# Performance work log

Measured on AMD Instinct MI355X. Metric: run time of the kernel, lower is better.

Reference implementation:

```python
import jax, jax.numpy as jnp
import numpy as np

D, H = 2048, 16
Q_RANK, KV_RANK = 1536, 512
NOPE, ROPE_D, V_D = 128, 64, 128
QK_D = NOPE + ROPE_D  # 192
S, B = 2048, 1
THETA = 10000.0
EPS = 1e-5


def rmsnorm(x, w, eps=EPS):
    return x * jax.lax.rsqrt(jnp.mean(x * x, -1, keepdims=True) + eps) * w


def rope_cos_sin(s, d, theta=THETA):
    inv = 1.0 / (theta ** (jnp.arange(0, d, 2, dtype=jnp.float32) / d))
    f = jnp.arange(s, dtype=jnp.float32)[:, None] * inv[None, :]  # [s, d//2]
    emb = jnp.concatenate([f, f], -1)  # [s, d]
    return jnp.cos(emb), jnp.sin(emb)


def apply_rope(x, cos, sin):
    # DeepSeek-V3 variant: de-interleave consecutive pairs into [even | odd] halves first
    b, h, s, d = x.shape
    x = x.reshape(b, h, s, d // 2, 2).transpose(0, 1, 2, 4, 3).reshape(b, h, s, d)
    x1, x2 = jnp.split(x, 2, -1)
    rot = jnp.concatenate([-x2, x1], -1)
    return x * cos + rot * sin


def setup_inputs() -> dict:
    key = jax.random.key(0)
    ks = jax.random.split(key, 10)
    s = 0.02
    return {
        "x": jax.random.normal(ks[0], (S, B, D), jnp.float32),
        "norm1_w": jnp.ones((D,), jnp.float32),
        "q_a_w": jax.random.normal(ks[1], (D, Q_RANK), jnp.float32) * s,
        "q_a_ln_w": jnp.ones((Q_RANK,), jnp.float32),
        "q_b_w": jax.random.normal(ks[2], (Q_RANK, H * QK_D), jnp.float32) * s,
        "kv_a_w": jax.random.normal(ks[3], (D, KV_RANK + ROPE_D), jnp.float32) * s,
        "kv_a_ln_w": jnp.ones((KV_RANK,), jnp.float32),
        "kv_b_w": jax.random.normal(ks[4], (KV_RANK, H * (NOPE + V_D)), jnp.float32) * s,
        "o_w": jax.random.normal(ks[5], (H * V_D, D), jnp.float32) * s,
        "norm2_w": jnp.ones((D,), jnp.float32),
        "ffn_w1": jax.random.normal(ks[6], (D, 4 * D), jnp.float32) * s,
        "ffn_b1": jnp.zeros((4 * D,), jnp.float32),
        "ffn_w2": jax.random.normal(ks[7], (4 * D, D), jnp.float32) * s,
        "ffn_b2": jnp.zeros((D,), jnp.float32),
    }


def reference(x, norm1_w, q_a_w, q_a_ln_w, q_b_w, kv_a_w, kv_a_ln_w, kv_b_w, o_w,
              norm2_w, ffn_w1, ffn_b1, ffn_w2, ffn_b2):
    # x: [S, B, D] (block transposes to [B, S, D] before MLA)
    hs = jnp.swapaxes(rmsnorm(x, norm1_w), 0, 1)  # [B, S, D]
    b, s, _ = hs.shape

    # --- MLA: low-rank Q and KV with decoupled RoPE ---
    q = rmsnorm(hs @ q_a_w, q_a_ln_w) @ q_b_w                    # [B, S, H*192]
    q = q.reshape(b, s, H, QK_D).transpose(0, 2, 1, 3)           # [B, H, S, 192]
    q_nope, q_pe = q[..., :NOPE], q[..., NOPE:]

    kv_a = hs @ kv_a_w                                           # [B, S, 576]
    c_kv, k_pe = kv_a[..., :KV_RANK], kv_a[..., KV_RANK:]        # [B,S,512], [B,S,64]
    kv = rmsnorm(c_kv, kv_a_ln_w) @ kv_b_w                       # [B, S, H*256]
    kv = kv.reshape(b, s, H, NOPE + V_D).transpose(0, 2, 1, 3)   # [B, H, S, 256]
    k_nope, v = kv[..., :NOPE], kv[..., NOPE:]

    cos, sin = rope_cos_sin(s, ROPE_D)
    q_pe = apply_rope(q_pe, cos, sin)                            # [B, H, S, 64]
    k_pe = apply_rope(k_pe[:, None, :, :], cos, sin)             # [B, 1, S, 64]

    q_full = jnp.concatenate([q_nope, q_pe], -1)                 # [B, H, S, 192]
    k_full = jnp.concatenate([k_nope, jnp.broadcast_to(k_pe, (b, H, s, ROPE_D))], -1)

    scores = jnp.einsum('bhqd,bhkd->bhqk', q_full, k_full) * (1.0 / np.sqrt(QK_D))
    causal = jnp.tril(jnp.ones((s, s), bool))
    scores = jnp.where(causal, scores, jnp.finfo(scores.dtype).min)
    attn = jax.nn.softmax(scores, -1)
    out = jnp.einsum('bhqk,bhkd->bhqd', attn, v)                 # [B, H, S, 128]
    out = out.transpose(0, 2, 1, 3).reshape(b, s, H * V_D) @ o_w # [B, S, D]

    x = x + jnp.swapaxes(out, 0, 1)                              # residual, back to [S,B,D]

    # --- FFN (exact GELU) ---
    h2 = rmsnorm(x, norm2_w)
    ffn = jax.nn.gelu(h2 @ ffn_w1 + ffn_b1, approximate=False) @ ffn_w2 + ffn_b2
    return x + ffn
```

## Files before the change

### kernel.cpp

```cpp
#include <hip/hip_runtime.h>
#include <hip/hip_bf16.h>

typedef __hip_bfloat16 bf16;
using bf16x8 = __attribute__((ext_vector_type(8))) __bf16;
using f32x4  = __attribute__((ext_vector_type(4))) float;

#define S_   2048
#define D_   2048
#define H_   16
#define QR_  1536
#define KVR_ 512
#define NOPE_ 128
#define ROPE_ 64
#define VD_  128
#define QKD_ 192
#define EPS_ 1e-5f
#define QKVN 2112

#define GLDS16(g, l) \
    __builtin_amdgcn_global_load_lds((const __attribute__((address_space(1))) void*)(g), \
                                     (__attribute__((address_space(3))) void*)(l), 16, 0, 0)

#define PIPE_WAIT4 asm volatile("s_waitcnt vmcnt(4)\n\ts_barrier" ::: "memory")
#define PIPE_WAIT0 asm volatile("s_waitcnt vmcnt(0)\n\ts_barrier" ::: "memory")

__global__ __launch_bounds__(256) void gemm_k(
    const bf16* __restrict__ A, const bf16* __restrict__ BT, void* __restrict__ Cv,
    const float* __restrict__ bias, const float* __restrict__ res,
    int M, int N, int K, int lda, int ldb, int ldc,
    long long strideA, long long strideB, long long strideC,
    int mode, int causal, int ksplit, int kchunk)
{
    int bn = blockIdx.x, bm = blockIdx.y;
    int bzC = blockIdx.z;
    int bz = bzC, kc = 0;
    if (ksplit > 1) { kc = bzC % ksplit; bz = bzC / ksplit; }
    if (causal == 1 && bn > bm) return;
    A  += (size_t)bz * strideA;
    BT += (size_t)bz * strideB;

    int k_end = K;
    if (causal == 2) { int kl = (bm + 1) * 128; if (kl < k_end) k_end = kl; }
    int k_begin = kc * kchunk;
    if (k_begin + kchunk < k_end) k_end = k_begin + kchunk;
    if (k_begin >= k_end) return;
    int nIter = (k_end - k_begin) >> 5;

    __shared__ bf16 sA[3 * 128 * 32];
    __shared__ bf16 sB[3 * 128 * 32];

    int tid  = threadIdx.x;
    int lane = tid & 63, wave = tid >> 6;
    int wr = wave >> 1, wc = wave & 1;
    int fr = lane & 15, fq = lane >> 4;

    int row0 = bm * 128, col0 = bn * 128;

    int srow = wave * 16 + (lane >> 2);
    int sko  = (lane & 3) * 8;
    const bf16* ga0 = A + (size_t)(row0 + srow) * lda + sko;
    const bf16* ga1 = ga0 + (size_t)64 * lda;
    int bn0 = col0 + srow;      if (bn0 > N - 1) bn0 = N - 1;
    int bn1 = col0 + srow + 64; if (bn1 > N - 1) bn1 = N - 1;
    const bf16* gb0 = BT + (size_t)bn0 * ldb + sko;
    const bf16* gb1 = BT + (size_t)bn1 * ldb + sko;
    bf16* lA0 = &sA[(wave * 16) * 32];
    bf16* lA1 = &sA[(64 + wave * 16) * 32];
    bf16* lB0 = &sB[(wave * 16) * 32];
    bf16* lB1 = &sB[(64 + wave * 16) * 32];

#define STAGE(ofs, k0) do {                  \
        GLDS16(ga0 + (k0), lA0 + (ofs));     \
        GLDS16(ga1 + (k0), lA1 + (ofs));     \
        GLDS16(gb0 + (k0), lB0 + (ofs));     \
        GLDS16(gb1 + (k0), lB1 + (ofs));     \
    } while (0)

    f32x4 acc[4][4] = {};

#define COMPUTE(ofs) do {                                                           \
        bf16x8 af[4], bv[4];                                                        \
        _Pragma("unroll")                                                           \
        for (int i = 0; i < 4; ++i)                                                 \
            af[i] = *(const bf16x8*)&sA[(ofs) + (wr*64 + i*16 + fr)*32 + fq*8];     \
        _Pragma("unroll")                                                           \
        for (int j = 0; j < 4; ++j)                                                 \
            bv[j] = *(const bf16x8*)&sB[(ofs) + (wc*64 + j*16 + fr)*32 + fq*8];     \
        _Pragma("unroll")                                                           \
        for (int i = 0; i < 4; ++i)                                                 \
            _Pragma("unroll")                                                       \
            for (int j = 0; j < 4; ++j)                                             \
                acc[i][j] = __builtin_amdgcn_mfma_f32_16x16x32_bf16(af[i], bv[j], acc[i][j], 0, 0, 0); \
    } while (0)

    STAGE(0, k_begin);
    if (nIter > 1) STAGE(4096, k_begin + 32);

    int curo = 0, pfo = 8192;
    int it = 0;
    for (; it < nIter - 1; ++it) {
        PIPE_WAIT4;
        if (it + 2 < nIter) STAGE(pfo, k_begin + (it + 2) * 32);
        COMPUTE(curo);
        curo += 4096; if (curo == 12288) curo = 0;
        pfo  += 4096; if (pfo  == 12288) pfo  = 0;
    }
    PIPE_WAIT0;
    COMPUTE(curo);
#undef STAGE
#undef COMPUTE

    #pragma unroll
    for (int i = 0; i < 4; ++i) {
        #pragma unroll
        for (int j = 0; j < 4; ++j) {
            int gc = col0 + wc*64 + j*16 + fr;
            if (gc >= N) continue;
            #pragma unroll
            for (int r = 0; r < 4; ++r) {
                int gr = row0 + wr*64 + i*16 + fq*4 + r;
                float v = acc[i][j][r];
                size_t off = (size_t)bzC * strideC + (size_t)gr * ldc + gc;
                if (mode == 0 || mode == 6) {
                    ((float*)Cv)[off] = v;
                } else if (mode == 1) {
                    ((bf16*)Cv)[off] = __float2bfloat16(v);
                } else if (mode == 2) {
                    ((float*)Cv)[off] = v + res[(size_t)gr * ldc + gc];
                } else if (mode == 3) {
                    float t = v + bias[gc];
                    t = 0.5f * t * (1.0f + erff(t * 0.70710678118654752f));
                    ((bf16*)Cv)[off] = __float2bfloat16(t);
                } else {
                    ((float*)Cv)[off] = v + bias[gc] + res[(size_t)gr * ldc + gc];
                }
            }
        }
    }
}

__global__ __launch_bounds__(256) void red_k(const float* __restrict__ part,
        long long pstride4, int nch, const float* __restrict__ res,
        const float* __restrict__ bias, long long cols4,
        float* __restrict__ dstF, bf16* __restrict__ dstB, long long n4)
{
    long long i = (long long)blockIdx.x * 256 + threadIdx.x;
    long long stride = (long long)gridDim.x * 256;
    for (; i < n4; i += stride) {
        float4 v = ((const float4*)part)[i];
        for (int k = 1; k < nch; ++k) {
            float4 p = ((const float4*)part)[i + k * pstride4];
            v.x += p.x; v.y += p.y; v.z += p.z; v.w += p.w;
        }
        if (res) {
            float4 rr = ((const float4*)res)[i];
            v.x += rr.x; v.y += rr.y; v.z += rr.z; v.w += rr.w;
        }
        if (bias) {
            float4 b = ((const float4*)bias)[i % cols4];
            v.x += b.x; v.y += b.y; v.z += b.z; v.w += b.w;
        }
        if (dstB) {
            ushort4 o;
            bf16 t0 = __float2bfloat16(v.x); o.x = *(unsigned short*)&t0;
            bf16 t1 = __float2bfloat16(v.y); o.y = *(unsigned short*)&t1;
            bf16 t2 = __float2bfloat16(v.z); o.z = *(unsigned short*)&t2;
            bf16 t3 = __float2bfloat16(v.w); o.w = *(unsigned short*)&t3;
            ((ushort4*)dstB)[i] = o;
        } else {
            ((float4*)dstF)[i] = v;
        }
    }
}

__global__ __launch_bounds__(128) void pv_red(const float* __restrict__ part,
                                              bf16* __restrict__ ao, int grp)
{
    int r = blockIdx.x, head = blockIdx.y, d = threadIdx.x;
    int nv = ((r >> 7) + 4) >> 2;
    const float* p = part + ((size_t)head * 4) * S_ * VD_ + (size_t)r * VD_ + d;
    float s = 0.f;
    for (int k = 0; k < nv; ++k) s += p[(size_t)k * S_ * VD_];
    ao[(size_t)r * (H_ * VD_) + grp * 1024 + head * VD_ + d] = __float2bfloat16(s);
}

__global__ __launch_bounds__(256) void transpose_w(const float* __restrict__ in,
                                                   bf16* __restrict__ out, int R, int C)
{
    __shared__ float t[32][33];
    int c0 = blockIdx.x * 32, r0 = blockIdx.y * 32;
    int tx = threadIdx.x, ty = threadIdx.y;
    for (int j = ty; j < 32; j += 8) {
        int r = r0 + j, c = c0 + tx;
        t[j][tx] = (r < R && c < C) ? in[(size_t)r * C + c] : 0.f;
    }
    __syncthreads();
    for (int j = ty; j < 32; j += 8) {
        int c = c0 + j, r = r0 + tx;
        if (c < C && r < R) out[(size_t)c * R + r] = __float2bfloat16(t[tx][j]);
    }
}

__global__ __launch_bounds__(256) void transpose_v(const bf16* __restrict__ kv,
                                                   bf16* __restrict__ vT)
{
    __shared__ bf16 t[32][33];
    int h = blockIdx.z;
    int d0 = blockIdx.x * 32, s0 = blockIdx.y * 32;
    int tx = threadIdx.x, ty = threadIdx.y;
    for (int j = ty; j < 32; j += 8)
        t[j][tx] = kv[(size_t)(s0 + j) * (H_*256) + h*256 + 128 + d0 + tx];
    __syncthreads();
    for (int j = ty; j < 32; j += 8)
        vT[((size_t)h * VD_ + d0 + j) * S_ + s0 + tx] = t[tx][j];
}

__global__ __launch_bounds__(256) void rmsnorm_k(const float* __restrict__ in,
                                                 const float* __restrict__ w,
                                                 bf16* __restrict__ out,
                                                 int cols, int istride, int ostride)
{
    int row = blockIdx.x, tid = threadIdx.x;
    const float* ip = in + (size_t)row * istride;
    bf16* op = out + (size_t)row * ostride;
    float ss = 0.f;
    for (int c = tid; c < cols; c += 256) { float v = ip[c]; ss = fmaf(v, v, ss); }
    for (int o = 32; o > 0; o >>= 1) ss += __shfl_down(ss, o, 64);
    __shared__ float red[4];
    __shared__ float s_sc;
    int wave = tid >> 6, lane = tid & 63;
    if (lane == 0) red[wave] = ss;
    __syncthreads();
    if (tid == 0) s_sc = rsqrtf((red[0]+red[1]+red[2]+red[3]) / (float)cols + EPS_);
    __syncthreads();
    float sc = s_sc;
    for (int c = tid; c < cols; c += 256)
        op[c] = __float2bfloat16(ip[c] * sc * w[c]);
}

#define ROPE_LC 0.28782313662425575f

__global__ __launch_bounds__(192) void build_q(const bf16* __restrict__ q,
                                               bf16* __restrict__ qf)
{
    int s = blockIdx.x, h = blockIdx.y, t = threadIdx.x;
    const float scale = 0.07216878364870323f;
    const bf16* src = q + (size_t)s * (H_*QKD_) + h * QKD_;
    bf16* dst = qf + ((size_t)h * S_ + s) * QKD_;
    if (t < NOPE_) {
        dst[t] = __float2bfloat16(__bfloat162float(src[t]) * scale);
    } else {
        int i = (t - NOPE_) & 31;
        bool hi = (t - NOPE_) >= 32;
        float a = __bfloat162float(src[NOPE_ + 2*i]);
        float b = __bfloat162float(src[NOPE_ + 2*i + 1]);
        float inv = __expf(-(float)i * ROPE_LC);
        float f = (float)s * inv, c, sn;
        sincosf(f, &sn, &c);
        float v = hi ? (b * c + a * sn) : (a * c - b * sn);
        dst[t] = __float2bfloat16(v * scale);
    }
}

__global__ __launch_bounds__(192) void build_k(const bf16* __restrict__ kv,
                                               const float* __restrict__ qakva32,
                                               bf16* __restrict__ kf)
{
    int s = blockIdx.x, h = blockIdx.y, t = threadIdx.x;
    const bf16* src = kv + (size_t)s * (H_*256) + h * 256;
    bf16* dst = kf + ((size_t)h * S_ + s) * QKD_;
    if (t < NOPE_) {
        dst[t] = src[t];
    } else {
        int i = (t - NOPE_) & 31;
        bool hi = (t - NOPE_) >= 32;
        const float* pe = qakva32 + (size_t)s * QKVN + (QR_ + KVR_);
        float a = pe[2*i], b = pe[2*i + 1];
        float inv = __expf(-(float)i * ROPE_LC);
        float f = (float)s * inv, c, sn;
        sincosf(f, &sn, &c);
        dst[t] = __float2bfloat16(hi ? (b * c + a * sn) : (a * c - b * sn));
    }
}

__global__ __launch_bounds__(256) void softmax_k(bf16* __restrict__ Sc)
{
    int q = blockIdx.x, h = blockIdx.y;
    bf16* row = Sc + ((size_t)h * S_ + q) * S_;
    int n = q + 1;
    int klim = ((q >> 7) + 1) << 7;
    int tid = threadIdx.x, lane = tid & 63, wave = tid >> 6;
    __shared__ float red[4];
    __shared__ float bc;

    float v[8];
    #pragma unroll
    for (int k = 0; k < 8; ++k) {
        int c = tid + k * 256;
        v[k] = (c < n) ? __bfloat162float(row[c]) : -3.0e38f;
    }
    float mx = v[0];
    #pragma unroll
    for (int k = 1; k < 8; ++k) mx = fmaxf(mx, v[k]);
    for (int o = 32; o > 0; o >>= 1) mx = fmaxf(mx, __shfl_down(mx, o, 64));
    if (lane == 0) red[wave] = mx;
    __syncthreads();
    if (tid == 0) bc = fmaxf(fmaxf(red[0], red[1]), fmaxf(red[2], red[3]));
    __syncthreads();
    float m = bc;
    float sum = 0.f;
    #pragma unroll
    for (int k = 0; k < 8; ++k) {
        int c = tid + k * 256;
        v[k] = (c < n) ? __expf(v[k] - m) : 0.f;
        sum += v[k];
    }
    for (int o = 32; o > 0; o >>= 1) sum += __shfl_down(sum, o, 64);
    __syncthreads();
    if (lane == 0) red[wave] = sum;
    __syncthreads();
    if (tid == 0) bc = 1.0f / (red[0] + red[1] + red[2] + red[3]);
    __syncthreads();
    float inv = bc;
    #pragma unroll
    for (int k = 0; k < 8; ++k) {
        int c = tid + k * 256;
        if (c < klim) row[c] = __float2bfloat16(c < n ? v[k] * inv : 0.f);
    }
}

static inline void gemm(hipStream_t st, const bf16* A, const bf16* BT, void* C,
                        const float* bias, const float* res,
                        int M, int N, int K, int lda, int ldb, int ldc,
                        long long sA, long long sB, long long sC,
                        int batch, int mode, int causal, int ksplit = 1, int kchunk = 0)
{
    if (kchunk == 0) kchunk = K;
    dim3 g((N + 127) / 128, M / 128, batch * ksplit);
    gemm_k<<<g, 256, 0, st>>>(A, BT, C, bias, res, M, N, K, lda, ldb, ldc,
                              sA, sB, sC, mode, causal, ksplit, kchunk);
}

static inline void transw(hipStream_t st, const float* in, bf16* out, int R, int C)
{
    dim3 g((C + 31) / 32, (R + 31) / 32);
    transpose_w<<<g, dim3(32, 8), 0, st>>>(in, out, R, C);
}

extern "C" void kernel_launch(void* const* d_in, const int* in_sizes, int n_in,
                              void* d_out, int out_size, void* d_ws, size_t ws_size,
                              hipStream_t stream)
{
    const float* x        = (const float*)d_in[0];
    const float* norm1_w  = (const float*)d_in[1];
    const float* q_a_w    = (const float*)d_in[2];
    const float* q_a_ln_w = (const float*)d_in[3];
    const float* q_b_w    = (const float*)d_in[4];
    const float* kv_a_w   = (const float*)d_in[5];
    const float* kv_a_ln_w= (const float*)d_in[6];
    const float* kv_b_w   = (const float*)d_in[7];
    const float* o_w      = (const float*)d_in[8];
    const float* norm2_w  = (const float*)d_in[9];
    const float* ffn_w1   = (const float*)d_in[10];
    const float* ffn_b1   = (const float*)d_in[11];
    const float* ffn_w2   = (const float*)d_in[12];
    const float* ffn_b2   = (const float*)d_in[13];
    float* out = (float*)d_out;

    size_t off = 0;
    auto alloc = [&](size_t bytes) -> void* {
        void* p = (char*)d_ws + off;
        off += (bytes + 255) & ~(size_t)255;
        return p;
    };
    bf16*  hs     = (bf16*) alloc((size_t)S_*D_*2);
    bf16*  wqakvT = (bf16*) alloc((size_t)QKVN*D_*2);
    bf16*  wqbT   = (bf16*) alloc((size_t)(H_*QKD_)*QR_*2);
    bf16*  wkvbT  = (bf16*) alloc((size_t)(H_*(NOPE_+VD_))*KVR_*2);
    bf16*  woT    = (bf16*) alloc((size_t)D_*(H_*VD_)*2);
    bf16*  wf1T   = (bf16*) alloc((size_t)(4*D_)*D_*2);
    bf16*  wf2T   = (bf16*) alloc((size_t)D_*(4*D_)*2);
    float* qakva32= (float*)alloc((size_t)S_*QKVN*4);
    bf16*  qln    = (bf16*) alloc((size_t)S_*QR_*2);
    bf16*  kvln   = (bf16*) alloc((size_t)S_*KVR_*2);
    bf16*  qb     = (bf16*) alloc((size_t)S_*H_*QKD_*2);
    bf16*  kvb    = (bf16*) alloc((size_t)S_*H_*(NOPE_+VD_)*2);
    bf16*  qf     = (bf16*) alloc((size_t)H_*S_*QKD_*2);
    bf16*  kf     = (bf16*) alloc((size_t)H_*S_*QKD_*2);
    bf16*  vT     = (bf16*) alloc((size_t)H_*VD_*S_*2);
    bf16*  Sc     = (bf16*) alloc((size_t)8*S_*S_*2);
    float* qakvaP = (float*)Sc;
    float* qbP    = (float*)Sc;
    float* pvP    = (float*)qakva32;
    float* oP     = (float*)qf;
    float* f2P    = (float*)qf;
    float* x2     = qakva32;
    bf16*  h2     = qb;
    bf16*  ao     = kvb;
    bf16*  a1     = Sc;

    transw(stream, q_a_w,  wqakvT,                    D_,  QR_);
    transw(stream, kv_a_w, wqakvT + (size_t)QR_ * D_, D_,  KVR_+ROPE_);
    transw(stream, q_b_w,  wqbT,  QR_, H_*QKD_);
    transw(stream, kv_b_w, wkvbT, KVR_, H_*(NOPE_+VD_));
    transw(stream, o_w,    woT,   H_*VD_, D_);
    transw(stream, ffn_w1, wf1T,  D_,  4*D_);
    transw(stream, ffn_w2, wf2T,  4*D_, D_);

    rmsnorm_k<<<S_, 256, 0, stream>>>(x, norm1_w, hs, D_, D_, D_);

    gemm(stream, hs, wqakvT, qakvaP, nullptr, nullptr, S_, QKVN, D_, D_, D_, QKVN,
         0, 0, (long long)S_*QKVN, 1, 6, 0, 2, 1024);
    red_k<<<1024, 256, 0, stream>>>(qakvaP, (long long)S_*QKVN/4, 2, nullptr, nullptr, 1,
                                    qakva32, nullptr, (long long)S_*QKVN/4);

    rmsnorm_k<<<S_, 256, 0, stream>>>(qakva32, q_a_ln_w, qln, QR_, QKVN, QR_);
    gemm(stream, qln, wqbT, qbP, nullptr, nullptr, S_, H_*QKD_, QR_, QR_, QR_, H_*QKD_,
         0, 0, (long long)S_*(H_*QKD_), 1, 6, 0, 2, 768);
    red_k<<<1024, 256, 0, stream>>>(qbP, (long long)S_*(H_*QKD_)/4, 2, nullptr, nullptr, 1,
                                    nullptr, qb, (long long)S_*(H_*QKD_)/4);

    rmsnorm_k<<<S_, 256, 0, stream>>>(qakva32 + QR_, kv_a_ln_w, kvln, KVR_, QKVN, KVR_);
    gemm(stream, kvln, wkvbT, kvb, nullptr, nullptr, S_, H_*(NOPE_+VD_), KVR_,
         KVR_, KVR_, H_*(NOPE_+VD_), 0, 0, 0, 1, 1, 0);

    build_q<<<dim3(S_, H_), 192, 0, stream>>>(qb, qf);
    build_k<<<dim3(S_, H_), 192, 0, stream>>>(kvb, qakva32, kf);
    transpose_v<<<dim3(VD_/32, S_/32, H_), dim3(32, 8), 0, stream>>>(kvb, vT);

    for (int g = 0; g < 2; ++g) {
        const bf16* qfg = qf + (size_t)g * 8 * S_ * QKD_;
        const bf16* kfg = kf + (size_t)g * 8 * S_ * QKD_;
        const bf16* vTg = vT + (size_t)g * 8 * VD_ * S_;
        gemm(stream, qfg, kfg, Sc, nullptr, nullptr,
             S_, S_, QKD_, QKD_, QKD_, S_,
             (long long)S_*QKD_, (long long)S_*QKD_, (long long)S_*S_, 8, 1, 1);
        softmax_k<<<dim3(S_, 8), 256, 0, stream>>>(Sc);
        gemm(stream, Sc, vTg, pvP, nullptr, nullptr,
             S_, VD_, S_, S_, S_, VD_,
             (long long)S_*S_, (long long)VD_*S_, (long long)S_*VD_, 8, 6, 2, 4, 512);
        pv_red<<<dim3(S_, 8), 128, 0, stream>>>(pvP, ao, g);
    }

    gemm(stream, ao, woT, oP, nullptr, nullptr, S_, D_, H_*VD_, H_*VD_, H_*VD_, D_,
         0, 0, (long long)S_*D_, 1, 6, 0, 2, 1024);
    red_k<<<1024, 256, 0, stream>>>(oP, (long long)S_*D_/4, 2, x, nullptr, 1,
                                    x2, nullptr, (long long)S_*D_/4);

    rmsnorm_k<<<S_, 256, 0, stream>>>(x2, norm2_w, h2, D_, D_, D_);
    gemm(stream, h2, wf1T, a1, ffn_b1, nullptr, S_, 4*D_, D_, D_, D_, 4*D_,
         0, 0, 0, 1, 3, 0);
    gemm(stream, a1, wf2T, f2P, nullptr, nullptr, S_, D_, 4*D_, 4*D_, 4*D_, D_,
         0, 0, (long long)S_*D_, 1, 6, 0, 2, 4096);
    red_k<<<1024, 256, 0, stream>>>(f2P, (long long)S_*D_/4, 2, x2, ffn_b2, D_/4,
                                    out, nullptr, (long long)S_*D_/4);
}
```

Before: 973.2 us.

## Add 256x256-tile 8-wave MFMA GEMM kernel for dense projections

Adds a new GEMM kernel with 256x256 output tiles, 512 threads, double-buffered direct-to-LDS loads with XOR swizzle, and interleaved load/MFMA phases using setprio. The dense projection GEMMs (QKV-A, Q-B, output, both FFN layers) now use it, with split-K factors and partial-buffer placements adjusted. The aim is higher arithmetic intensity and better MFMA utilisation per block. In exchange, grids are smaller (fewer blocks for 2048-row problems), and split-K reductions read more partial buffers.

```diff
diff --git a/kernel.cpp b/kernel.cpp
--- a/kernel.cpp
+++ b/kernel.cpp
@@ -139,6 +139,157 @@
     }
 }
 
+__global__ __launch_bounds__(512, 2) void gemm256_k(
+    const bf16* __restrict__ A, const bf16* __restrict__ BT, void* __restrict__ Cv,
+    const float* __restrict__ bias,
+    int M, int N, int K, int lda, int ldb, int ldc,
+    long long strideC, int mode, int kchunk)
+{
+    int bn = blockIdx.x, bm = blockIdx.y, kc = blockIdx.z;
+    int k_begin = kc * kchunk;
+    int k_end = (k_begin + kchunk < K) ? (k_begin + kchunk) : K;
+    int NT = (k_end - k_begin) >> 6;
+
+    __shared__ __align__(16) bf16 sA[2 * 256 * 64];
+    __shared__ __align__(16) bf16 sB[2 * 256 * 64];
+
+    int tid = threadIdx.x;
+    int lane = tid & 63, w = tid >> 6;
+    int wr = w >> 2, wc = w & 3;
+    int fr = lane & 15, fq = lane >> 4;
+    int row0 = bm * 256, col0 = bn * 256;
+
+    int g0 = tid, g1 = tid + 512;
+    int r0 = g0 >> 3, l0 = (g0 & 7) ^ (r0 & 7);
+    int r1 = g1 >> 3, l1 = (g1 & 7) ^ (r1 & 7);
+    const bf16* gA00 = A + (size_t)(row0 + r0) * lda + k_begin + l0 * 8;
+    const bf16* gA01 = A + (size_t)(row0 + r1) * lda + k_begin + l1 * 8;
+    const bf16* gA10 = gA00 + (size_t)128 * lda;
+    const bf16* gA11 = gA01 + (size_t)128 * lda;
+    int c00 = col0 + r0;       if (c00 > N - 1) c00 = N - 1;
+    int c01 = col0 + r1;       if (c01 > N - 1) c01 = N - 1;
+    int c10 = col0 + 128 + r0; if (c10 > N - 1) c10 = N - 1;
+    int c11 = col0 + 128 + r1; if (c11 > N - 1) c11 = N - 1;
+    const bf16* gB00 = BT + (size_t)c00 * ldb + k_begin + l0 * 8;
+    const bf16* gB01 = BT + (size_t)c01 * ldb + k_begin + l1 * 8;
+    const bf16* gB10 = BT + (size_t)c10 * ldb + k_begin + l0 * 8;
+    const bf16* gB11 = BT + (size_t)c11 * ldb + k_begin + l1 * 8;
+
+#define ST_HALF(arr, bofs, p0, p1, t) do {                                  \
+        GLDS16((p0) + (size_t)(t) * 64, (arr) + (bofs) + w * 512);          \
+        GLDS16((p1) + (size_t)(t) * 64, (arr) + (bofs) + w * 512 + 4096);   \
+    } while (0)
+#define ST_A0(b, t) ST_HALF(sA, (b) * 16384,        gA00, gA01, t)
+#define ST_A1(b, t) ST_HALF(sA, (b) * 16384 + 8192, gA10, gA11, t)
+#define ST_B0(b, t) ST_HALF(sB, (b) * 16384,        gB00, gB01, t)
+#define ST_B1(b, t) ST_HALF(sB, (b) * 16384 + 8192, gB10, gB11, t)
+
+    int arow = (wr * 128 + fr) * 64;
+    int brow = (wc * 64 + fr) * 64;
+    int pk0 = (fq ^ (fr & 7)) * 8;
+    int pk1 = pk0 ^ 32;
+
+    f32x4 acc[8][4] = {};
+
+#define MFMA_QUAD(AF, IOFF, N0) do {                                        \
+        __builtin_amdgcn_s_setprio(1);                                      \
+        _Pragma("unroll")                                                   \
+        for (int m = 0; m < 4; ++m) {                                       \
+            _Pragma("unroll")                                               \
+            for (int n = 0; n < 2; ++n) {                                   \
+                acc[(IOFF)+m][(N0)+n] = __builtin_amdgcn_mfma_f32_16x16x32_bf16( \
+                    AF[m][0], bfr[(N0)+n][0], acc[(IOFF)+m][(N0)+n], 0, 0, 0);   \
+                acc[(IOFF)+m][(N0)+n] = __builtin_amdgcn_mfma_f32_16x16x32_bf16( \
+                    AF[m][1], bfr[(N0)+n][1], acc[(IOFF)+m][(N0)+n], 0, 0, 0);   \
+            }                                                               \
+        }                                                                   \
+        __builtin_amdgcn_s_setprio(0);                                      \
+    } while (0)
+
+    ST_A0(0, 0); ST_A1(0, 0); ST_B0(0, 0); ST_B1(0, 0);
+    if (NT > 1) { ST_B0(1, 1); ST_B1(1, 1); ST_A0(1, 1); }
+    if (NT > 1) asm volatile("s_waitcnt vmcnt(6)" ::: "memory");
+    else        asm volatile("s_waitcnt vmcnt(0)" ::: "memory");
+    __builtin_amdgcn_s_barrier();
+
+    for (int t = 0; t < NT; ++t) {
+        int buf = t & 1;
+        int sbase = buf * 16384;
+        bf16x8 aflo[4][2], afhi[4][2], bfr[4][2];
+
+        #pragma unroll
+        for (int m = 0; m < 4; ++m) {
+            aflo[m][0] = *(const bf16x8*)&sA[sbase + arow + m*1024 + pk0];
+            aflo[m][1] = *(const bf16x8*)&sA[sbase + arow + m*1024 + pk1];
+        }
+        #pragma unroll
+        for (int n = 0; n < 4; ++n) {
+            bfr[n][0] = *(const bf16x8*)&sB[sbase + brow + n*1024 + pk0];
+            bfr[n][1] = *(const bf16x8*)&sB[sbase + brow + n*1024 + pk1];
+        }
+        if (t + 1 < NT) ST_A1((t + 1) & 1, t + 1);
+        __builtin_amdgcn_s_barrier();
+        asm volatile("s_waitcnt lgkmcnt(0)" ::: "memory");
+        __builtin_amdgcn_sched_barrier(0);
+        MFMA_QUAD(aflo, 0, 0);
+        __builtin_amdgcn_s_barrier();
+
+        #pragma unroll
+        for (int m = 0; m < 4; ++m) {
+            afhi[m][0] = *(const bf16x8*)&sA[sbase + arow + 4096 + m*1024 + pk0];
+            afhi[m][1] = *(const bf16x8*)&sA[sbase + arow + 4096 + m*1024 + pk1];
+        }
+        if (t + 2 < NT) ST_B0(buf, t + 2);
+        __builtin_amdgcn_s_barrier();
+        MFMA_QUAD(aflo, 0, 2);
+        __builtin_amdgcn_s_barrier();
+
+        if (t + 2 < NT) ST_B1(buf, t + 2);
+        __builtin_amdgcn_s_barrier();
+        asm volatile("s_waitcnt lgkmcnt(0)" ::: "memory");
+        __builtin_amdgcn_sched_barrier(0);
+        MFMA_QUAD(afhi, 4, 0);
+        __builtin_amdgcn_s_barrier();
+
+        if (t + 2 < NT) ST_A0(buf, t + 2);
+        if (t < NT - 2) asm volatile("s_waitcnt vmcnt(6)" ::: "memory");
+        else            asm volatile("s_waitcnt vmcnt(0)" ::: "memory");
+        __builtin_amdgcn_s_barrier();
+        MFMA_QUAD(afhi, 4, 2);
+        __builtin_amdgcn_s_barrier();
+    }
+#undef MFMA_QUAD
+#undef ST_A0
+#undef ST_A1
+#undef ST_B0
+#undef ST_B1
+#undef ST_HALF
+
+    #pragma unroll
+    for (int i = 0; i < 8; ++i) {
+        #pragma unroll
+        for (int j = 0; j < 4; ++j) {
+            int gc = col0 + wc*64 + j*16 + fr;
+            if (gc >= N) continue;
+            #pragma unroll
+            for (int r = 0; r < 4; ++r) {
+                int gr = row0 + wr*128 + i*16 + fq*4 + r;
+                float v = acc[i][j][r];
+                size_t off = (size_t)kc * strideC + (size_t)gr * ldc + gc;
+                if (mode == 0 || mode == 6) {
+                    ((float*)Cv)[off] = v;
+                } else if (mode == 1) {
+                    ((bf16*)Cv)[off] = __float2bfloat16(v);
+                } else {
+                    float tt = v + bias[gc];
+                    tt = 0.5f * tt * (1.0f + erff(tt * 0.70710678118654752f));
+                    ((bf16*)Cv)[off] = __float2bfloat16(tt);
+                }
+            }
+        }
+    }
+}
+
 __global__ __launch_bounds__(256) void red_k(const float* __restrict__ part,
         long long pstride4, int nch, const float* __restrict__ res,
         const float* __restrict__ bias, long long cols4,
@@ -339,6 +490,17 @@
     dim3 g((N + 127) / 128, M / 128, batch * ksplit);
     gemm_k<<<g, 256, 0, st>>>(A, BT, C, bias, res, M, N, K, lda, ldb, ldc,
                               sA, sB, sC, mode, causal, ksplit, kchunk);
+}
+
+static inline void gemm256(hipStream_t st, const bf16* A, const bf16* BT, void* C,
+                           const float* bias, int M, int N, int K,
+                           int lda, int ldb, int ldc, long long sC,
+                           int mode, int ksplit = 1, int kchunk = 0)
+{
+    if (kchunk == 0) kchunk = K;
+    dim3 g((N + 255) / 256, M / 256, ksplit);
+    gemm256_k<<<g, 512, 0, st>>>(A, BT, C, bias, M, N, K, lda, ldb, ldc,
+                                 sC, mode, kchunk);
 }
 
 static inline void transw(hipStream_t st, const float* in, bf16* out, int R, int C)
@@ -392,8 +554,8 @@
     float* qakvaP = (float*)Sc;
     float* qbP    = (float*)Sc;
     float* pvP    = (float*)qakva32;
-    float* oP     = (float*)qf;
-    float* f2P    = (float*)qf;
+    float* oP     = (float*)Sc;
+    float* f2P    = (float*)d_ws;
     float* x2     = qakva32;
     bf16*  h2     = qb;
     bf16*  ao     = kvb;
@@ -409,14 +571,14 @@
 
     rmsnorm_k<<<S_, 256, 0, stream>>>(x, norm1_w, hs, D_, D_, D_);
 
-    gemm(stream, hs, wqakvT, qakvaP, nullptr, nullptr, S_, QKVN, D_, D_, D_, QKVN,
-         0, 0, (long long)S_*QKVN, 1, 6, 0, 2, 1024);
-    red_k<<<1024, 256, 0, stream>>>(qakvaP, (long long)S_*QKVN/4, 2, nullptr, nullptr, 1,
+    gemm256(stream, hs, wqakvT, qakvaP, nullptr, S_, QKVN, D_, D_, D_, QKVN,
+            (long long)S_*QKVN, 6, 3, 768);
+    red_k<<<1024, 256, 0, stream>>>(qakvaP, (long long)S_*QKVN/4, 3, nullptr, nullptr, 1,
                                     qakva32, nullptr, (long long)S_*QKVN/4);
 
     rmsnorm_k<<<S_, 256, 0, stream>>>(qakva32, q_a_ln_w, qln, QR_, QKVN, QR_);
-    gemm(stream, qln, wqbT, qbP, nullptr, nullptr, S_, H_*QKD_, QR_, QR_, QR_, H_*QKD_,
-         0, 0, (long long)S_*(H_*QKD_), 1, 6, 0, 2, 768);
+    gemm256(stream, qln, wqbT, qbP, nullptr, S_, H_*QKD_, QR_, QR_, QR_, H_*QKD_,
+            (long long)S_*(H_*QKD_), 6, 2, 768);
     red_k<<<1024, 256, 0, stream>>>(qbP, (long long)S_*(H_*QKD_)/4, 2, nullptr, nullptr, 1,
                                     nullptr, qb, (long long)S_*(H_*QKD_)/4);
 
@@ -442,16 +604,16 @@
         pv_red<<<dim3(S_, 8), 128, 0, stream>>>(pvP, ao, g);
     }
 
-    gemm(stream, ao, woT, oP, nullptr, nullptr, S_, D_, H_*VD_, H_*VD_, H_*VD_, D_,
-         0, 0, (long long)S_*D_, 1, 6, 0, 2, 1024);
-    red_k<<<1024, 256, 0, stream>>>(oP, (long long)S_*D_/4, 2, x, nullptr, 1,
+    gemm256(stream, ao, woT, oP, nullptr, S_, D_, H_*VD_, H_*VD_, H_*VD_, D_,
+            (long long)S_*D_, 6, 4, 512);
+    red_k<<<1024, 256, 0, stream>>>(oP, (long long)S_*D_/4, 4, x, nullptr, 1,
                                     x2, nullptr, (long long)S_*D_/4);
 
     rmsnorm_k<<<S_, 256, 0, stream>>>(x2, norm2_w, h2, D_, D_, D_);
-    gemm(stream, h2, wf1T, a1, ffn_b1, nullptr, S_, 4*D_, D_, D_, D_, 4*D_,
-         0, 0, 0, 1, 3, 0);
-    gemm(stream, a1, wf2T, f2P, nullptr, nullptr, S_, D_, 4*D_, 4*D_, 4*D_, D_,
-         0, 0, (long long)S_*D_, 1, 6, 0, 2, 4096);
-    red_k<<<1024, 256, 0, stream>>>(f2P, (long long)S_*D_/4, 2, x2, ffn_b2, D_/4,
+    gemm256(stream, h2, wf1T, a1, ffn_b1, S_, 4*D_, D_, D_, D_, 4*D_,
+            0, 3, 1, 0);
+    gemm256(stream, a1, wf2T, f2P, nullptr, S_, D_, 4*D_, 4*D_, 4*D_, D_,
+            (long long)S_*D_, 6, 4, 2048);
+    red_k<<<1024, 256, 0, stream>>>(f2P, (long long)S_*D_/4, 4, x2, ffn_b2, D_/4,
                                     out, nullptr, (long long)S_*D_/4);
 }
```

Result: faster. 946.7 us (-2.7%).
